# Optimization experiments

Measured on AMD Instinct MI355X. Metric: run time of the kernel, lower is better.

## Reference

```python
import jax, jax.numpy as jnp
import numpy as np

N, K, H, X_DIM, S_DIM = 50000, 8, 128, 32, 27
LSTM_IN = X_DIM + 3 * H  # 416


def setup_inputs() -> dict:
    key = jax.random.key(0)
    ks = jax.random.split(key, 16)

    def u(k, shape, fan_in):
        lim = 1.0 / np.sqrt(fan_in)
        return jax.random.uniform(k, shape, jnp.float32, -lim, lim)

    return {
        "x": jax.random.normal(ks[0], (N, X_DIM), jnp.float32),
        "h_self": jax.random.normal(ks[1], (N, H), jnp.float32),
        "c_self": jax.random.normal(ks[2], (N, H), jnp.float32),
        "h_inflows": jax.random.normal(ks[3], (N, K, H), jnp.float32),
        "inflow_valid": jax.random.randint(ks[4], (N, K), 0, 2) > 0,
        "static": jax.random.normal(ks[5], (N, S_DIM), jnp.float32),
        # Linear weights stored (out, in) as in eqx.nn.Linear
        "Wn": u(ks[6], (H, H), H),                     # W_neighbor, no bias
        "Wg": u(ks[7], (H, 2 * H), 2 * H),             # W_inflow_gate
        "bg": u(ks[8], (H,), 2 * H),
        "Ws": u(ks[9], (H, S_DIM), S_DIM),             # W_static
        "bs": u(ks[10], (H,), S_DIM),
        "Wl": u(ks[11], (4 * H, LSTM_IN), LSTM_IN),    # W_lstm
        "bl": u(ks[12], (4 * H,), LSTM_IN),
        "ln_w": jnp.ones((H,), jnp.float32),           # ln_h affine
        "ln_b": jnp.zeros((H,), jnp.float32),
    }


def reference(x, h_self, c_self, h_inflows, inflow_valid, static,
              Wn, Wg, bg, Ws, bs, Wl, bl, ln_w, ln_b):
    eps = 1e-5
    # per-neighbor message: [N,K,H]
    msgs = jnp.einsum('nkh,oh->nko', h_inflows, Wn)
    # inflow gate on concat(h_inflow, h_self): [N,K,H]
    h_tiled = jnp.broadcast_to(h_self[:, None, :], h_inflows.shape)
    gate_in = jnp.concatenate([h_inflows, h_tiled], axis=-1)  # [N,K,2H]
    gates = jax.nn.sigmoid(jnp.einsum('nkd,od->nko', gate_in, Wg) + bg)
    # masked sum over neighbors -> [N,H]
    mask = inflow_valid[..., None].astype(jnp.float32)
    neighbor_context = jnp.sum(gates * msgs * mask, axis=1)
    static_proj = static @ Ws.T + bs  # [N,H]
    combined = jnp.concatenate([x, h_self, neighbor_context, static_proj], axis=-1)
    z = combined @ Wl.T + bl  # [N,4H]
    i, f, o, g = jnp.split(z, 4, axis=-1)
    c_new = jax.nn.sigmoid(f) * c_self + jax.nn.sigmoid(i) * jnp.tanh(g)
    h_new = jax.nn.sigmoid(o) * jnp.tanh(c_new)
    # LayerNorm over hidden dim (eqx default eps=1e-5, affine)
    mu = jnp.mean(h_new, axis=-1, keepdims=True)
    var = jnp.mean(jnp.square(h_new - mu), axis=-1, keepdims=True)
    h_new = (h_new - mu) * jax.lax.rsqrt(var + eps) * ln_w + ln_b
    return (h_new, c_new)
```

## Files before the change

### kernel.cpp

```cpp
#include <hip/hip_runtime.h>
#include <hip/hip_bf16.h>

#define NN 50000
#define KI 8
#define H 128
#define XD 32
#define SD 27
#define CIN 416
#define CIN2 320
#define CPAD 328
#define ZOUT 512
#define NTILE_NB (NN / KI)
#define MB_LSTM 32
#define GRID_NB 1024

typedef __attribute__((ext_vector_type(8))) short bf16x8;
typedef __attribute__((ext_vector_type(4))) float f32x4;
typedef __attribute__((ext_vector_type(4))) unsigned short us4;

#define MFMA16(a, b, c) __builtin_amdgcn_mfma_f32_16x16x32_bf16((a), (b), (c), 0, 0, 0)

static __device__ __forceinline__ float sigmoidf_(float x) {
    return 1.0f / (1.0f + __expf(-x));
}
static __device__ __forceinline__ float tanhf_(float x) {
    return 1.0f - 2.0f / (__expf(2.0f * x) + 1.0f);
}
static __device__ __forceinline__ unsigned short bf(float f) {
    __hip_bfloat16 h = __float2bfloat16(f);
    return __builtin_bit_cast(unsigned short, h);
}
static __device__ __forceinline__ float dot4_(float4 a, float4 b) {
    return a.x * b.x + a.y * b.y + a.z * b.z + a.w * b.w;
}

__global__ __launch_bounds__(256) void k_prep(
    const float* __restrict__ Wn, const float* __restrict__ Wg,
    const float* __restrict__ Wl, const float* __restrict__ bl,
    const float* __restrict__ Ws, const float* __restrict__ bs,
    unsigned short* __restrict__ WnB, unsigned short* __restrict__ WgB,
    unsigned short* __restrict__ WpB, float* __restrict__ bp)
{
    const int b = blockIdx.x, t = threadIdx.x;
    if (b < 512) {
        const float* wr = Wl + (size_t)b * CIN;
        unsigned short* out = WpB + (size_t)b * CIN2;
        for (int c = t; c < CIN2; c += 256) {
            float v;
            if (c < 288) v = wr[c];
            else if (c < 288 + SD) {
                int s = c - 288;
                float acc = 0.f;
                for (int j = 0; j < H; ++j) acc += wr[288 + j] * Ws[j * SD + s];
                v = acc;
            } else v = 0.f;
            out[c] = bf(v);
        }
        if (t == 0) {
            float acc = bl[b];
            for (int j = 0; j < H; ++j) acc += wr[288 + j] * bs[j];
            bp[b] = acc;
        }
    } else {
        int idx = (b - 512) * 256 + t;
        for (int r = idx; r < 49152; r += 16384) {
            if (r < 16384) WnB[r] = bf(Wn[r]);
            else WgB[r - 16384] = bf(Wg[r - 16384]);
        }
    }
}

__global__ __launch_bounds__(256, 2) void k_nb_mfma(
    const float* __restrict__ hself_g, const float* __restrict__ hin_g,
    const unsigned char* __restrict__ valid_raw,
    const unsigned short* __restrict__ WnB, const unsigned short* __restrict__ WgB,
    const float* __restrict__ bg,
    unsigned short* __restrict__ ncb, int nc_stride)
{
    __shared__ unsigned short hin_s[64 * 128];
    __shared__ unsigned short hs_s[8 * 128];
    __shared__ float gh_s[8][128];
    __shared__ unsigned short ncs[8 * 128];
    __shared__ float valid_s[64];

    const int t = threadIdx.x;
    const int w = t >> 6, l = t & 63;
    const int ln = l & 15, lk = l >> 4;

    int det = 0;
    #pragma unroll
    for (int i = 0; i < 64; ++i) det |= valid_raw[4 * i + 1];
    const bool f8 = (det != 0);

    bf16x8 Bn[2][4], Ba[2][4], Bb[2][4];
    const int cbase = w * 32;
    #pragma unroll
    for (int c = 0; c < 2; ++c) {
        const int col = cbase + c * 16 + ln;
        #pragma unroll
        for (int kk = 0; kk < 4; ++kk) {
            const int k0 = kk * 32 + lk * 8;
            Bn[c][kk] = *(const bf16x8*)(WnB + col * H + k0);
            Ba[c][kk] = *(const bf16x8*)(WgB + col * 2 * H + k0);
            Bb[c][kk] = *(const bf16x8*)(WgB + col * 2 * H + H + k0);
        }
    }
    const float bg0 = bg[cbase + ln];
    const float bg1 = bg[cbase + 16 + ln];

    for (int tile = blockIdx.x; tile < NTILE_NB; tile += GRID_NB) {
        const int nb = tile * 8;

        if (t < 64)
            valid_s[t] = (f8 ? (valid_raw[(size_t)nb * KI + t] != 0)
                             : (((const unsigned int*)valid_raw)[(size_t)nb * KI + t] != 0u))
                             ? 1.f : 0.f;
        {
            const float4* src = (const float4*)(hin_g + (size_t)nb * KI * H);
            float4 r0[8];
            #pragma unroll
            for (int i = 0; i < 8; ++i) r0[i] = src[t + i * 256];
            float4 hv = ((const float4*)(hself_g + (size_t)nb * H))[t];
            #pragma unroll
            for (int i = 0; i < 8; ++i) {
                int e = (t + i * 256) * 4, row = e >> 7, col = e & 127;
                unsigned byte = (unsigned)(row * 256 + col * 2) ^ (unsigned)((row & 7) << 4);
                us4 pk = { bf(r0[i].x), bf(r0[i].y), bf(r0[i].z), bf(r0[i].w) };
                *(us4*)((char*)hin_s + byte) = pk;
            }
            {
                int e = t * 4, row = e >> 7, col = e & 127;
                unsigned byte = (unsigned)(row * 256 + col * 2) ^ (unsigned)((row & 7) << 4);
                us4 pk = { bf(hv.x), bf(hv.y), bf(hv.z), bf(hv.w) };
                *(us4*)((char*)hs_s + byte) = pk;
            }
        }
        __syncthreads();

        f32x4 accM[4][2], accP[4][2], accG[2];
        #pragma unroll
        for (int m = 0; m < 4; ++m)
            #pragma unroll
            for (int c = 0; c < 2; ++c) { accM[m][c] = (f32x4)0.f; accP[m][c] = (f32x4)0.f; }
        accG[0] = (f32x4)0.f; accG[1] = (f32x4)0.f;

        #pragma unroll
        for (int kk = 0; kk < 4; ++kk) {
            const int k0 = kk * 32 + lk * 8;
            bf16x8 am[4];
            #pragma unroll
            for (int m = 0; m < 4; ++m) {
                int row = m * 16 + ln;
                unsigned byte = (unsigned)(row * 256 + k0 * 2) ^ (unsigned)((row & 7) << 4);
                am[m] = *(const bf16x8*)((const char*)hin_s + byte);
            }
            bf16x8 ah;
            {
                int row = ln & 7;
                unsigned byte = (unsigned)(row * 256 + k0 * 2) ^ (unsigned)((row & 7) << 4);
                ah = *(const bf16x8*)((const char*)hs_s + byte);
            }
            #pragma unroll
            for (int m = 0; m < 4; ++m)
                #pragma unroll
                for (int c = 0; c < 2; ++c) {
                    accM[m][c] = MFMA16(am[m], Bn[c][kk], accM[m][c]);
                    accP[m][c] = MFMA16(am[m], Ba[c][kk], accP[m][c]);
                }
            accG[0] = MFMA16(ah, Bb[0][kk], accG[0]);
            accG[1] = MFMA16(ah, Bb[1][kk], accG[1]);
        }

        #pragma unroll
        for (int c = 0; c < 2; ++c)
            #pragma unroll
            for (int r = 0; r < 4; ++r) {
                int row = lk * 4 + r;
                if (row < 8) gh_s[row][cbase + c * 16 + ln] = accG[c][r];
            }
        __syncthreads();

        #pragma unroll
        for (int m = 0; m < 4; ++m) {
            const int node = 2 * m + (lk >> 1);
            #pragma unroll
            for (int c = 0; c < 2; ++c) {
                const int col = cbase + c * 16 + ln;
                const float bgc = c ? bg1 : bg0;
                const float ghv = gh_s[node][col];
                float sum = 0.f;
                #pragma unroll
                for (int r = 0; r < 4; ++r) {
                    int row = m * 16 + lk * 4 + r;
                    float g = sigmoidf_(accP[m][c][r] + ghv + bgc);
                    sum += valid_s[row] * g * accM[m][c][r];
                }
                sum += __shfl_xor(sum, 16);
                if ((l & 16) == 0) ncs[(2 * m + (l >> 5)) * H + col] = bf(sum);
            }
        }
        __syncthreads();

        {
            int e = t * 4, node = e >> 7, col = e & 127;
            us4 v = *(const us4*)(ncs + e);
            *(us4*)(ncb + (size_t)(nb + node) * nc_stride + col) = v;
        }
    }
}

__global__ __launch_bounds__(512, 4) void k_lstm_mfma(
    const float* __restrict__ x_g, const float* __restrict__ hself_g,
    const float* __restrict__ cself_g, const float* __restrict__ stat_g,
    const unsigned short* __restrict__ ncb, int nc_stride,
    const unsigned short* __restrict__ WpB, const float* __restrict__ bp,
    const float* __restrict__ lnw, const float* __restrict__ lnb,
    float* __restrict__ h_out, float* __restrict__ c_out)
{
    __shared__ char smem[MB_LSTM * CPAD * 2];
    unsigned short* comb = (unsigned short*)smem;
    float (*hpre)[132] = (float(*)[132])smem;

    const int t = threadIdx.x;
    const int nb = blockIdx.x * MB_LSTM;
    const int w = t >> 6, l = t & 63, ln = l & 15, lk = l >> 4;
    const int hcol = w * 16 + ln;

    if (t < 256) {
        int e = t * 4, row = e >> 5, col = e & 31;
        us4 pk = { 0, 0, 0, 0 };
        if (nb + row < NN) {
            float4 v = ((const float4*)(x_g + (size_t)nb * XD))[t];
            pk = us4{ bf(v.x), bf(v.y), bf(v.z), bf(v.w) };
        }
        *(us4*)(comb + row * CPAD + col) = pk;
    }
    #pragma unroll
    for (int i = 0; i < 2; ++i) {
        int p4 = t + i * 512;
        int e = p4 * 4, row = e >> 7, col = 32 + (e & 127);
        us4 pk = { 0, 0, 0, 0 };
        if (nb + row < NN) {
            float4 v = ((const float4*)(hself_g + (size_t)nb * H))[p4];
            pk = us4{ bf(v.x), bf(v.y), bf(v.z), bf(v.w) };
        }
        *(us4*)(comb + row * CPAD + col) = pk;
    }
    #pragma unroll
    for (int i = 0; i < 2; ++i) {
        int p4 = t + i * 512;
        int e = p4 * 4, row = e >> 7, col = e & 127;
        us4 v = { 0, 0, 0, 0 };
        if (nb + row < NN) v = *(const us4*)(ncb + (size_t)(nb + row) * nc_stride + col);
        *(us4*)(comb + row * CPAD + 160 + col) = v;
    }
    for (int i = t; i < MB_LSTM * SD; i += 512) {
        int row = i / SD, col = i - row * SD;
        unsigned short v = 0;
        if (nb + row < NN) v = bf(stat_g[(size_t)(nb + row) * SD + col]);
        comb[row * CPAD + 288 + col] = v;
    }
    if (t < MB_LSTM * 5) {
        int row = t / 5, col = 315 + t % 5;
        comb[row * CPAD + col] = 0;
    }

    float cpre[8];
    #pragma unroll
    for (int m = 0; m < 2; ++m)
        #pragma unroll
        for (int r = 0; r < 4; ++r) {
            int node = m * 16 + lk * 4 + r;
            size_t n = (size_t)(nb + node);
            cpre[m * 4 + r] = (n < NN) ? cself_g[n * H + hcol] : 0.f;
        }
    __syncthreads();

    f32x4 acc[2][4];
    #pragma unroll
    for (int m = 0; m < 2; ++m)
        #pragma unroll
        for (int g = 0; g < 4; ++g) acc[m][g] = (f32x4)0.f;

    #pragma unroll
    for (int kk = 0; kk < 10; ++kk) {
        const int k0 = kk * 32 + lk * 8;
        bf16x8 a0 = *(const bf16x8*)(comb + ln * CPAD + k0);
        bf16x8 a1 = *(const bf16x8*)(comb + (16 + ln) * CPAD + k0);
        #pragma unroll
        for (int g = 0; g < 4; ++g) {
            bf16x8 b = *(const bf16x8*)(WpB + (size_t)(g * H + hcol) * CIN2 + k0);
            acc[0][g] = MFMA16(a0, b, acc[0][g]);
            acc[1][g] = MFMA16(a1, b, acc[1][g]);
        }
    }
    __syncthreads();

    {
        const float bi = bp[hcol], bff = bp[H + hcol];
        const float bo = bp[2 * H + hcol], bgg = bp[3 * H + hcol];
        #pragma unroll
        for (int m = 0; m < 2; ++m)
            #pragma unroll
            for (int r = 0; r < 4; ++r) {
                int node = m * 16 + lk * 4 + r;
                size_t n = (size_t)(nb + node);
                if (n < NN) {
                    float zi = acc[m][0][r] + bi;
                    float zf = acc[m][1][r] + bff;
                    float zo = acc[m][2][r] + bo;
                    float zg = acc[m][3][r] + bgg;
                    float cn = sigmoidf_(zf) * cpre[m * 4 + r] + sigmoidf_(zi) * tanhf_(zg);
                    c_out[n * H + hcol] = cn;
                    hpre[node][hcol] = sigmoidf_(zo) * tanhf_(cn);
                }
            }
    }
    __syncthreads();

    #pragma unroll
    for (int jj = 0; jj < 4; ++jj) {
        const int j = w * 4 + jj;
        const size_t n = (size_t)(nb + j);
        if (n < NN) {
            float a = hpre[j][l];
            float b = hpre[j][64 + l];
            float s = a + b, q = a * a + b * b;
            #pragma unroll
            for (int off = 1; off < 64; off <<= 1) {
                s += __shfl_xor(s, off);
                q += __shfl_xor(q, off);
            }
            float mu = s * (1.0f / 128.0f);
            float var = q * (1.0f / 128.0f) - mu * mu;
            float rstd = rsqrtf(var + 1e-5f);
            h_out[n * H + l]      = (a - mu) * rstd * lnw[l] + lnb[l];
            h_out[n * H + 64 + l] = (b - mu) * rstd * lnw[64 + l] + lnb[64 + l];
        }
    }
}

__global__ __launch_bounds__(256) void k_nb_f32(
    const float* __restrict__ hself_g, const float* __restrict__ hin_g,
    const unsigned char* __restrict__ valid_raw,
    const float* __restrict__ Wn, const float* __restrict__ Wg,
    const float* __restrict__ bg, float* __restrict__ nc)
{
    __shared__ float4 hin_s[8 * KI * (H / 4)];
    __shared__ float4 hs_s[8 * (H / 4)];
    __shared__ int flag8;
    const int t = threadIdx.x;
    const int nb = blockIdx.x * 8;
    {
        int loc = 0;
        if (t < 64) {
            #pragma unroll
            for (int i = 0; i < 16; ++i) loc |= valid_raw[4 * (t * 16 + i) + 1];
        }
        int any = __any(loc != 0);
        if (t == 0) flag8 = any;
    }
    const float4* src_hin = (const float4*)(hin_g + (size_t)nb * KI * H);
    #pragma unroll
    for (int i = 0; i < 8; ++i) hin_s[t + i * 256] = src_hin[t + i * 256];
    hs_s[t] = ((const float4*)(hself_g + (size_t)nb * H))[t];
    __syncthreads();
    const int o = t & 127, g = t >> 7;
    float msg[4][KI], gat[4][KI], gh[4];
    #pragma unroll
    for (int j = 0; j < 4; ++j) {
        gh[j] = 0.f;
        #pragma unroll
        for (int k = 0; k < KI; ++k) { msg[j][k] = 0.f; gat[j][k] = 0.f; }
    }
    const float4* Wn4 = (const float4*)(Wn + (size_t)o * H);
    const float4* Wg4a = (const float4*)(Wg + (size_t)o * 2 * H);
    const float4* Wg4b = (const float4*)(Wg + (size_t)o * 2 * H + H);
    for (int d4 = 0; d4 < H / 4; ++d4) {
        float4 wn = Wn4[d4], w0 = Wg4a[d4], w1 = Wg4b[d4];
        #pragma unroll
        for (int j = 0; j < 4; ++j) {
            const int node = g * 4 + j;
            gh[j] += dot4_(w1, hs_s[node * 32 + d4]);
            #pragma unroll
            for (int k = 0; k < KI; ++k) {
                float4 hv = hin_s[(node * KI + k) * 32 + d4];
                msg[j][k] += dot4_(wn, hv);
                gat[j][k] += dot4_(w0, hv);
            }
        }
    }
    const float bgo = bg[o];
    const unsigned int* valid32 = (const unsigned int*)valid_raw;
    const int f8 = flag8;
    #pragma unroll
    for (int j = 0; j < 4; ++j) {
        const int n = nb + g * 4 + j;
        float acc = 0.f;
        #pragma unroll
        for (int k = 0; k < KI; ++k) {
            bool v = f8 ? (valid_raw[n * KI + k] != 0) : (valid32[n * KI + k] != 0u);
            if (v) acc += sigmoidf_(gat[j][k] + gh[j] + bgo) * msg[j][k];
        }
        nc[(size_t)n * H + o] = acc;
    }
}

__global__ __launch_bounds__(256) void k_lstm_f32(
    const float* __restrict__ x_g, const float* __restrict__ hself_g,
    const float* __restrict__ cself_g, const float* __restrict__ stat_g,
    const float* __restrict__ nc,
    const float* __restrict__ Ws, const float* __restrict__ bs,
    const float* __restrict__ Wl, const float* __restrict__ bl,
    const float* __restrict__ lnw, const float* __restrict__ lnb,
    float* __restrict__ h_out, float* __restrict__ c_out)
{
    __shared__ float4 comb4[16 * (CIN / 4)];
    __shared__ float zsh[16 * ZOUT];
    __shared__ float stat_s[16 * SD];
    float* combf = (float*)comb4;
    const int t = threadIdx.x;
    const int nb = blockIdx.x * 16;
    #pragma unroll
    for (int i = 0; i < 2; ++i) {
        int idx = t + i * 256;
        combf[(idx >> 5) * CIN + (idx & 31)] = x_g[(size_t)nb * XD + idx];
    }
    #pragma unroll
    for (int i = 0; i < 8; ++i) {
        int idx = t + i * 256;
        combf[(idx >> 7) * CIN + 32 + (idx & 127)] = hself_g[(size_t)nb * H + idx];
    }
    #pragma unroll
    for (int i = 0; i < 8; ++i) {
        int idx = t + i * 256;
        combf[(idx >> 7) * CIN + 160 + (idx & 127)] = nc[(size_t)nb * H + idx];
    }
    stat_s[t] = stat_g[(size_t)nb * SD + t];
    if (t < 16 * SD - 256) stat_s[t + 256] = stat_g[(size_t)nb * SD + t + 256];
    __syncthreads();
    {
        const int o = t & 127, jg = t >> 7;
        #pragma unroll
        for (int jj = 0; jj < 8; ++jj) {
            const int j = jg * 8 + jj;
            float s = bs[o];
            #pragma unroll
            for (int c = 0; c < SD; ++c) s += Ws[o * SD + c] * stat_s[j * SD + c];
            combf[j * CIN + 288 + o] = s;
        }
    }
    __syncthreads();
    float acc0[16], acc1[16];
    #pragma unroll
    for (int j = 0; j < 16; ++j) { acc0[j] = 0.f; acc1[j] = 0.f; }
    const float4* W0 = (const float4*)(Wl + (size_t)t * CIN);
    const float4* W1 = (const float4*)(Wl + (size_t)(t + 256) * CIN);
    for (int d4 = 0; d4 < CIN / 4; ++d4) {
        float4 w0 = W0[d4], w1 = W1[d4];
        #pragma unroll
        for (int j = 0; j < 16; ++j) {
            float4 cv = comb4[j * (CIN / 4) + d4];
            acc0[j] += dot4_(w0, cv);
            acc1[j] += dot4_(w1, cv);
        }
    }
    const float bl0 = bl[t], bl1 = bl[t + 256];
    #pragma unroll
    for (int j = 0; j < 16; ++j) {
        zsh[j * ZOUT + t] = acc0[j] + bl0;
        zsh[j * ZOUT + 256 + t] = acc1[j] + bl1;
    }
    __syncthreads();
    {
        const int h = t & 127, jg = t >> 7;
        #pragma unroll
        for (int jj = 0; jj < 8; ++jj) {
            const int j = jg * 8 + jj;
            const size_t n = (size_t)(nb + j);
            float zi = zsh[j * ZOUT + h];
            float zf = zsh[j * ZOUT + 128 + h];
            float zo = zsh[j * ZOUT + 256 + h];
            float zg = zsh[j * ZOUT + 384 + h];
            float cn = sigmoidf_(zf) * cself_g[n * H + h] + sigmoidf_(zi) * tanhf(zg);
            c_out[n * H + h] = cn;
            zsh[j * ZOUT + h] = sigmoidf_(zo) * tanhf(cn);
        }
    }
    __syncthreads();
    {
        const int w = t >> 6, lane = t & 63;
        #pragma unroll
        for (int jj = 0; jj < 4; ++jj) {
            const int j = w * 4 + jj;
            const size_t n = (size_t)(nb + j);
            float a = zsh[j * ZOUT + lane];
            float b = zsh[j * ZOUT + 64 + lane];
            float s = a + b, q = a * a + b * b;
            #pragma unroll
            for (int off = 1; off < 64; off <<= 1) {
                s += __shfl_xor(s, off);
                q += __shfl_xor(q, off);
            }
            float mu = s * (1.0f / 128.0f);
            float var = q * (1.0f / 128.0f) - mu * mu;
            float rstd = rsqrtf(var + 1e-5f);
            h_out[n * H + lane] = (a - mu) * rstd * lnw[lane] + lnb[lane];
            h_out[n * H + 64 + lane] = (b - mu) * rstd * lnw[64 + lane] + lnb[64 + lane];
        }
    }
}

extern "C" void kernel_launch(void* const* d_in, const int* in_sizes, int n_in,
                              void* d_out, int out_size, void* d_ws, size_t ws_size,
                              hipStream_t stream) {
    const float* x      = (const float*)d_in[0];
    const float* h_self = (const float*)d_in[1];
    const float* c_self = (const float*)d_in[2];
    const float* h_inf  = (const float*)d_in[3];
    const unsigned char* valid = (const unsigned char*)d_in[4];
    const float* statp  = (const float*)d_in[5];
    const float* Wn     = (const float*)d_in[6];
    const float* Wg     = (const float*)d_in[7];
    const float* bg     = (const float*)d_in[8];
    const float* Ws     = (const float*)d_in[9];
    const float* bs     = (const float*)d_in[10];
    const float* Wl     = (const float*)d_in[11];
    const float* bl     = (const float*)d_in[12];
    const float* lnw    = (const float*)d_in[13];
    const float* lnb    = (const float*)d_in[14];

    float* h_out = (float*)d_out;
    float* c_out = h_out + (size_t)NN * H;

    const size_t W_BYTES = (size_t)512 * CIN2 * 2 + 16384 * 2 + 32768 * 2 + 512 * 4;
    const size_t NC_BYTES = (size_t)NN * H * 2;

    if (ws_size >= W_BYTES) {
        char* p = (char*)d_ws;
        unsigned short* WpB = (unsigned short*)p;           p += (size_t)512 * CIN2 * 2;
        unsigned short* WnB = (unsigned short*)p;           p += 16384 * 2;
        unsigned short* WgB = (unsigned short*)p;           p += 32768 * 2;
        float* bp = (float*)p;                              p += 512 * 4;

        unsigned short* ncb;
        int nc_stride;
        if (ws_size >= W_BYTES + NC_BYTES + 64) {
            ncb = (unsigned short*)p;
            nc_stride = H;
        } else {
            ncb = (unsigned short*)h_out;
            nc_stride = 256;
        }

        k_prep<<<576, 256, 0, stream>>>(Wn, Wg, Wl, bl, Ws, bs,
                                        WnB, WgB, WpB, bp);
        k_nb_mfma<<<GRID_NB, 256, 0, stream>>>(h_self, h_inf, valid, WnB, WgB, bg,
                                               ncb, nc_stride);
        k_lstm_mfma<<<(NN + MB_LSTM - 1) / MB_LSTM, 512, 0, stream>>>(
            x, h_self, c_self, statp, ncb, nc_stride, WpB, bp,
            lnw, lnb, h_out, c_out);
    } else {
        float* nc_buf = (ws_size >= (size_t)NN * H * sizeof(float))
                            ? (float*)d_ws : h_out;
        k_nb_f32<<<NN / 8, 256, 0, stream>>>(h_self, h_inf, valid, Wn, Wg, bg, nc_buf);
        k_lstm_f32<<<NN / 16, 256, 0, stream>>>(x, h_self, c_self, statp, nc_buf,
                                                Ws, bs, Wl, bl, lnw, lnb, h_out, c_out);
    }
}
```

Measured before the change: 184.8 us.

## Double-buffer neighbor tiles with async global-to-LDS prefetch

The neighbor-gate kernel now prefetches the next tile's fp32 inflow states straight into a second LDS buffer with global_load_lds. It also loads that tile's h_self and validity mask while the current tile runs its MFMA work. The bf16 conversion moves from the staging store to the LDS read before each MFMA. The persistent grid is halved, and one barrier goes because each wave only reads its own gh_s columns. This trades twice the LDS footprint and fp32 LDS reads for overlap of global loads with compute, and it relies on correct waitcnt handling of the async LDS loads at the barrier.

```diff
diff --git a/kernel.cpp b/kernel.cpp
--- a/kernel.cpp
+++ b/kernel.cpp
@@ -12,13 +12,17 @@
 #define ZOUT 512
 #define NTILE_NB (NN / KI)
 #define MB_LSTM 32
-#define GRID_NB 1024
+#define GRID_NB 512
 
 typedef __attribute__((ext_vector_type(8))) short bf16x8;
 typedef __attribute__((ext_vector_type(4))) float f32x4;
 typedef __attribute__((ext_vector_type(4))) unsigned short us4;
+typedef __attribute__((ext_vector_type(8))) unsigned short us8;
 
 #define MFMA16(a, b, c) __builtin_amdgcn_mfma_f32_16x16x32_bf16((a), (b), (c), 0, 0, 0)
+
+typedef __attribute__((address_space(1))) const unsigned int gu32;
+typedef __attribute__((address_space(3))) unsigned int lu32;
 
 static __device__ __forceinline__ float sigmoidf_(float x) {
     return 1.0f / (1.0f + __expf(-x));
@@ -77,15 +81,16 @@
     const float* __restrict__ bg,
     unsigned short* __restrict__ ncb, int nc_stride)
 {
-    __shared__ unsigned short hin_s[64 * 128];
-    __shared__ unsigned short hs_s[8 * 128];
+    __shared__ __align__(16) float hinf[2][64 * 128];
+    __shared__ unsigned short hs_s[2][8 * 128];
     __shared__ float gh_s[8][128];
-    __shared__ unsigned short ncs[8 * 128];
-    __shared__ float valid_s[64];
+    __shared__ unsigned short ncs[2][8 * 128];
+    __shared__ float valid_s[2][64];
 
     const int t = threadIdx.x;
     const int w = t >> 6, l = t & 63;
     const int ln = l & 15, lk = l >> 4;
+    const int wb = __builtin_amdgcn_readfirstlane(w);
 
     int det = 0;
     #pragma unroll
@@ -108,34 +113,58 @@
     const float bg0 = bg[cbase + ln];
     const float bg1 = bg[cbase + 16 + ln];
 
+    int hin_off[8];
+    #pragma unroll
+    for (int i = 0; i < 8; ++i) {
+        int D = ((i * 4 + w) * 64 + l) * 16;
+        int row = D >> 9;
+        int inner = (D & 511) ^ ((row & 7) << 4);
+        hin_off[i] = row * 128 + (inner >> 2);
+    }
+
+    {
+        const size_t nb0 = (size_t)blockIdx.x * 8;
+        const float* hb = hin_g + nb0 * KI * H;
+        #pragma unroll
+        for (int i = 0; i < 8; ++i)
+            __builtin_amdgcn_global_load_lds((gu32*)(hb + hin_off[i]),
+                (lu32*)&hinf[0][(i * 4 + wb) * 256], 16, 0, 0);
+        float4 hv = ((const float4*)(hself_g + nb0 * H))[t];
+        {
+            int e = t * 4, row = e >> 7, col = e & 127;
+            unsigned byte = (unsigned)(row * 256 + col * 2) ^ (unsigned)((row & 7) << 4);
+            us4 pk = { bf(hv.x), bf(hv.y), bf(hv.z), bf(hv.w) };
+            *(us4*)((char*)hs_s[0] + byte) = pk;
+        }
+        if (t < 64)
+            valid_s[0][t] = (f8 ? (valid_raw[nb0 * KI + t] != 0)
+                                : (((const unsigned int*)valid_raw)[nb0 * KI + t] != 0u))
+                                ? 1.f : 0.f;
+    }
+    __syncthreads();
+
+    int p = 0;
     for (int tile = blockIdx.x; tile < NTILE_NB; tile += GRID_NB) {
         const int nb = tile * 8;
 
-        if (t < 64)
-            valid_s[t] = (f8 ? (valid_raw[(size_t)nb * KI + t] != 0)
-                             : (((const unsigned int*)valid_raw)[(size_t)nb * KI + t] != 0u))
-                             ? 1.f : 0.f;
-        {
-            const float4* src = (const float4*)(hin_g + (size_t)nb * KI * H);
-            float4 r0[8];
-            #pragma unroll
-            for (int i = 0; i < 8; ++i) r0[i] = src[t + i * 256];
-            float4 hv = ((const float4*)(hself_g + (size_t)nb * H))[t];
-            #pragma unroll
-            for (int i = 0; i < 8; ++i) {
-                int e = (t + i * 256) * 4, row = e >> 7, col = e & 127;
-                unsigned byte = (unsigned)(row * 256 + col * 2) ^ (unsigned)((row & 7) << 4);
-                us4 pk = { bf(r0[i].x), bf(r0[i].y), bf(r0[i].z), bf(r0[i].w) };
-                *(us4*)((char*)hin_s + byte) = pk;
-            }
-            {
-                int e = t * 4, row = e >> 7, col = e & 127;
-                unsigned byte = (unsigned)(row * 256 + col * 2) ^ (unsigned)((row & 7) << 4);
-                us4 pk = { bf(hv.x), bf(hv.y), bf(hv.z), bf(hv.w) };
-                *(us4*)((char*)hs_s + byte) = pk;
-            }
-        }
-        __syncthreads();
+        const int next = tile + GRID_NB;
+        float4 hv;
+        unsigned vload = 0;
+        if (next < NTILE_NB) {
+            const size_t nnb = (size_t)next * 8;
+            const float* hb = hin_g + nnb * KI * H;
+            #pragma unroll
+            for (int i = 0; i < 8; ++i)
+                __builtin_amdgcn_global_load_lds((gu32*)(hb + hin_off[i]),
+                    (lu32*)&hinf[p ^ 1][(i * 4 + wb) * 256], 16, 0, 0);
+            hv = ((const float4*)(hself_g + nnb * H))[t];
+            if (t < 64)
+                vload = f8 ? (unsigned)valid_raw[nnb * KI + t]
+                           : ((const unsigned int*)valid_raw)[nnb * KI + t];
+        }
+
+        const float* hbuf = hinf[p];
+        const unsigned short* sbuf = hs_s[p];
 
         f32x4 accM[4][2], accP[4][2], accG[2];
         #pragma unroll
@@ -147,18 +176,21 @@
         #pragma unroll
         for (int kk = 0; kk < 4; ++kk) {
             const int k0 = kk * 32 + lk * 8;
-            bf16x8 am[4];
+            bf16x8 am[4], ah;
             #pragma unroll
             for (int m = 0; m < 4; ++m) {
-                int row = m * 16 + ln;
+                const int row = m * 16 + ln;
+                const unsigned x = (unsigned)((row & 7) << 4);
+                const float4 q0 = *(const float4*)((const char*)hbuf + row * 512 + ((k0 * 4) ^ x));
+                const float4 q1 = *(const float4*)((const char*)hbuf + row * 512 + ((k0 * 4 + 16) ^ x));
+                us8 pk = { bf(q0.x), bf(q0.y), bf(q0.z), bf(q0.w),
+                           bf(q1.x), bf(q1.y), bf(q1.z), bf(q1.w) };
+                am[m] = __builtin_bit_cast(bf16x8, pk);
+            }
+            {
+                const int row = ln & 7;
                 unsigned byte = (unsigned)(row * 256 + k0 * 2) ^ (unsigned)((row & 7) << 4);
-                am[m] = *(const bf16x8*)((const char*)hin_s + byte);
-            }
-            bf16x8 ah;
-            {
-                int row = ln & 7;
-                unsigned byte = (unsigned)(row * 256 + k0 * 2) ^ (unsigned)((row & 7) << 4);
-                ah = *(const bf16x8*)((const char*)hs_s + byte);
+                ah = *(const bf16x8*)((const char*)sbuf + byte);
             }
             #pragma unroll
             for (int m = 0; m < 4; ++m)
@@ -178,7 +210,6 @@
                 int row = lk * 4 + r;
                 if (row < 8) gh_s[row][cbase + c * 16 + ln] = accG[c][r];
             }
-        __syncthreads();
 
         #pragma unroll
         for (int m = 0; m < 4; ++m) {
@@ -193,19 +224,32 @@
                 for (int r = 0; r < 4; ++r) {
                     int row = m * 16 + lk * 4 + r;
                     float g = sigmoidf_(accP[m][c][r] + ghv + bgc);
-                    sum += valid_s[row] * g * accM[m][c][r];
+                    sum += valid_s[p][row] * g * accM[m][c][r];
                 }
                 sum += __shfl_xor(sum, 16);
-                if ((l & 16) == 0) ncs[(2 * m + (l >> 5)) * H + col] = bf(sum);
-            }
-        }
+                if ((l & 16) == 0) ncs[p][(2 * m + (l >> 5)) * H + col] = bf(sum);
+            }
+        }
+
+        if (next < NTILE_NB) {
+            int e = t * 4, row = e >> 7, col = e & 127;
+            unsigned byte = (unsigned)(row * 256 + col * 2) ^ (unsigned)((row & 7) << 4);
+            us4 pk = { bf(hv.x), bf(hv.y), bf(hv.z), bf(hv.w) };
+            *(us4*)((char*)hs_s[p ^ 1] + byte) = pk;
+            if (t < 64) {
+                bool v = f8 ? ((vload & 0xffu) != 0u) : (vload != 0u);
+                valid_s[p ^ 1][t] = v ? 1.f : 0.f;
+            }
+        }
+
         __syncthreads();
 
         {
             int e = t * 4, node = e >> 7, col = e & 127;
-            us4 v = *(const us4*)(ncs + e);
+            us4 v = *(const us4*)(ncs[p] + e);
             *(us4*)(ncb + (size_t)(nb + node) * nc_stride + col) = v;
         }
+        p ^= 1;
     }
 }
 
```

New measurement: 198.5 us. +7.4%, slower.

## Split neighbor kernel columns across eight waves to cut register pressure

Applied to the files above, without the earlier changes.

The neighbor-message kernel moves from 256 to 512 threads per block, with half as many blocks. Each wave now owns 16 output columns instead of 32, which halves the per-thread accumulators and resident weight fragments. The h_self gate weights are no longer held in registers; they are reloaded from global (cache) on each tile. One barrier is dropped because gh_s is now written and read by the same wave. The aim is higher occupancy and better latency hiding on the memory-bound h_inflows stream, at the cost of extra weight reloads and more threads idling during the h_self and output copy phases.

```diff
diff --git a/kernel.cpp b/kernel.cpp
--- a/kernel.cpp
+++ b/kernel.cpp
@@ -12,7 +12,7 @@
 #define ZOUT 512
 #define NTILE_NB (NN / KI)
 #define MB_LSTM 32
-#define GRID_NB 1024
+#define GRID_NB 512
 
 typedef __attribute__((ext_vector_type(8))) short bf16x8;
 typedef __attribute__((ext_vector_type(4))) float f32x4;
@@ -70,7 +70,7 @@
     }
 }
 
-__global__ __launch_bounds__(256, 2) void k_nb_mfma(
+__global__ __launch_bounds__(512, 4) void k_nb_mfma(
     const float* __restrict__ hself_g, const float* __restrict__ hin_g,
     const unsigned char* __restrict__ valid_raw,
     const unsigned short* __restrict__ WnB, const unsigned short* __restrict__ WgB,
@@ -92,21 +92,16 @@
     for (int i = 0; i < 64; ++i) det |= valid_raw[4 * i + 1];
     const bool f8 = (det != 0);
 
-    bf16x8 Bn[2][4], Ba[2][4], Bb[2][4];
-    const int cbase = w * 32;
-    #pragma unroll
-    for (int c = 0; c < 2; ++c) {
-        const int col = cbase + c * 16 + ln;
-        #pragma unroll
-        for (int kk = 0; kk < 4; ++kk) {
-            const int k0 = kk * 32 + lk * 8;
-            Bn[c][kk] = *(const bf16x8*)(WnB + col * H + k0);
-            Ba[c][kk] = *(const bf16x8*)(WgB + col * 2 * H + k0);
-            Bb[c][kk] = *(const bf16x8*)(WgB + col * 2 * H + H + k0);
-        }
-    }
-    const float bg0 = bg[cbase + ln];
-    const float bg1 = bg[cbase + 16 + ln];
+    bf16x8 Bn[4], Ba[4];
+    const int cbase = w * 16;
+    const int col = cbase + ln;
+    #pragma unroll
+    for (int kk = 0; kk < 4; ++kk) {
+        const int k0 = kk * 32 + lk * 8;
+        Bn[kk] = *(const bf16x8*)(WnB + col * H + k0);
+        Ba[kk] = *(const bf16x8*)(WgB + col * 2 * H + k0);
+    }
+    const float bg0 = bg[col];
 
     for (int tile = blockIdx.x; tile < NTILE_NB; tile += GRID_NB) {
         const int nb = tile * 8;
@@ -117,94 +112,82 @@
                              ? 1.f : 0.f;
         {
             const float4* src = (const float4*)(hin_g + (size_t)nb * KI * H);
-            float4 r0[8];
-            #pragma unroll
-            for (int i = 0; i < 8; ++i) r0[i] = src[t + i * 256];
-            float4 hv = ((const float4*)(hself_g + (size_t)nb * H))[t];
-            #pragma unroll
-            for (int i = 0; i < 8; ++i) {
-                int e = (t + i * 256) * 4, row = e >> 7, col = e & 127;
-                unsigned byte = (unsigned)(row * 256 + col * 2) ^ (unsigned)((row & 7) << 4);
+            float4 r0[4];
+            #pragma unroll
+            for (int i = 0; i < 4; ++i) r0[i] = src[t + i * 512];
+            float4 hv;
+            if (t < 256) hv = ((const float4*)(hself_g + (size_t)nb * H))[t];
+            #pragma unroll
+            for (int i = 0; i < 4; ++i) {
+                int e = (t + i * 512) * 4, row = e >> 7, c2 = e & 127;
+                unsigned byte = (unsigned)(row * 256 + c2 * 2) ^ (unsigned)((row & 7) << 4);
                 us4 pk = { bf(r0[i].x), bf(r0[i].y), bf(r0[i].z), bf(r0[i].w) };
                 *(us4*)((char*)hin_s + byte) = pk;
             }
-            {
-                int e = t * 4, row = e >> 7, col = e & 127;
-                unsigned byte = (unsigned)(row * 256 + col * 2) ^ (unsigned)((row & 7) << 4);
+            if (t < 256) {
+                int e = t * 4, row = e >> 7, c2 = e & 127;
+                unsigned byte = (unsigned)(row * 256 + c2 * 2) ^ (unsigned)((row & 7) << 4);
                 us4 pk = { bf(hv.x), bf(hv.y), bf(hv.z), bf(hv.w) };
                 *(us4*)((char*)hs_s + byte) = pk;
             }
         }
         __syncthreads();
 
-        f32x4 accM[4][2], accP[4][2], accG[2];
-        #pragma unroll
-        for (int m = 0; m < 4; ++m)
-            #pragma unroll
-            for (int c = 0; c < 2; ++c) { accM[m][c] = (f32x4)0.f; accP[m][c] = (f32x4)0.f; }
-        accG[0] = (f32x4)0.f; accG[1] = (f32x4)0.f;
+        f32x4 accM[4], accP[4], aG;
+        #pragma unroll
+        for (int m = 0; m < 4; ++m) { accM[m] = (f32x4)0.f; accP[m] = (f32x4)0.f; }
+        aG = (f32x4)0.f;
 
         #pragma unroll
         for (int kk = 0; kk < 4; ++kk) {
             const int k0 = kk * 32 + lk * 8;
-            bf16x8 am[4];
+            bf16x8 am[4], ah;
             #pragma unroll
             for (int m = 0; m < 4; ++m) {
                 int row = m * 16 + ln;
                 unsigned byte = (unsigned)(row * 256 + k0 * 2) ^ (unsigned)((row & 7) << 4);
                 am[m] = *(const bf16x8*)((const char*)hin_s + byte);
             }
-            bf16x8 ah;
             {
                 int row = ln & 7;
                 unsigned byte = (unsigned)(row * 256 + k0 * 2) ^ (unsigned)((row & 7) << 4);
                 ah = *(const bf16x8*)((const char*)hs_s + byte);
             }
-            #pragma unroll
-            for (int m = 0; m < 4; ++m)
-                #pragma unroll
-                for (int c = 0; c < 2; ++c) {
-                    accM[m][c] = MFMA16(am[m], Bn[c][kk], accM[m][c]);
-                    accP[m][c] = MFMA16(am[m], Ba[c][kk], accP[m][c]);
-                }
-            accG[0] = MFMA16(ah, Bb[0][kk], accG[0]);
-            accG[1] = MFMA16(ah, Bb[1][kk], accG[1]);
-        }
-
-        #pragma unroll
-        for (int c = 0; c < 2; ++c)
-            #pragma unroll
-            for (int r = 0; r < 4; ++r) {
-                int row = lk * 4 + r;
-                if (row < 8) gh_s[row][cbase + c * 16 + ln] = accG[c][r];
-            }
-        __syncthreads();
+            const bf16x8 bb = *(const bf16x8*)(WgB + col * 2 * H + H + k0);
+            #pragma unroll
+            for (int m = 0; m < 4; ++m) {
+                accM[m] = MFMA16(am[m], Bn[kk], accM[m]);
+                accP[m] = MFMA16(am[m], Ba[kk], accP[m]);
+            }
+            aG = MFMA16(ah, bb, aG);
+        }
+
+        #pragma unroll
+        for (int r = 0; r < 4; ++r) {
+            int row = lk * 4 + r;
+            if (row < 8) gh_s[row][col] = aG[r];
+        }
 
         #pragma unroll
         for (int m = 0; m < 4; ++m) {
             const int node = 2 * m + (lk >> 1);
-            #pragma unroll
-            for (int c = 0; c < 2; ++c) {
-                const int col = cbase + c * 16 + ln;
-                const float bgc = c ? bg1 : bg0;
-                const float ghv = gh_s[node][col];
-                float sum = 0.f;
-                #pragma unroll
-                for (int r = 0; r < 4; ++r) {
-                    int row = m * 16 + lk * 4 + r;
-                    float g = sigmoidf_(accP[m][c][r] + ghv + bgc);
-                    sum += valid_s[row] * g * accM[m][c][r];
-                }
-                sum += __shfl_xor(sum, 16);
-                if ((l & 16) == 0) ncs[(2 * m + (l >> 5)) * H + col] = bf(sum);
-            }
+            const float ghv = gh_s[node][col];
+            float sum = 0.f;
+            #pragma unroll
+            for (int r = 0; r < 4; ++r) {
+                int row = m * 16 + lk * 4 + r;
+                float g = sigmoidf_(accP[m][r] + ghv + bg0);
+                sum += valid_s[row] * g * accM[m][r];
+            }
+            sum += __shfl_xor(sum, 16);
+            if ((l & 16) == 0) ncs[(2 * m + (l >> 5)) * H + col] = bf(sum);
         }
         __syncthreads();
 
-        {
-            int e = t * 4, node = e >> 7, col = e & 127;
+        if (t < 256) {
+            int e = t * 4, node = e >> 7, c2 = e & 127;
             us4 v = *(const us4*)(ncs + e);
-            *(us4*)(ncb + (size_t)(nb + node) * nc_stride + col) = v;
+            *(us4*)(ncb + (size_t)(nb + node) * nc_stride + c2) = v;
         }
     }
 }
@@ -555,7 +538,7 @@
 
         k_prep<<<576, 256, 0, stream>>>(Wn, Wg, Wl, bl, Ws, bs,
                                         WnB, WgB, WpB, bp);
-        k_nb_mfma<<<GRID_NB, 256, 0, stream>>>(h_self, h_inf, valid, WnB, WgB, bg,
+        k_nb_mfma<<<GRID_NB, 512, 0, stream>>>(h_self, h_inf, valid, WnB, WgB, bg,
                                                ncb, nc_stride);
         k_lstm_mfma<<<(NN + MB_LSTM - 1) / MB_LSTM, 512, 0, stream>>>(
             x, h_self, c_self, statp, ncb, nc_stride, WpB, bp,
```

Measured after the change: 221.7 us. 1.2x slower.
